# Kernel tuning notes

Measured on AMD Instinct MI355X. Metric: run time of the kernel, lower is better.

Reference implementation:

```python
import jax, jax.numpy as jnp
import numpy as np

N = 6144      # nodes
D = 64        # per-side node feature dim (out_channels of prev layer)
FE = 32       # edge feature dim
E = 196608    # edges per sign (avg degree 32)
OUT = 64
IN_DIM = 4 * D + 4 * FE  # [pos_agg, neg_agg, x_1, x_2] + 4 pooled edge-feature groups


def _l2n(x):
    return x / jnp.maximum(jnp.linalg.norm(x, axis=-1, keepdims=True), 1e-12)


def _seg_mean(vals, idx, n):
    s = jax.ops.segment_sum(vals, idx, num_segments=n)
    c = jax.ops.segment_sum(jnp.ones((vals.shape[0], 1), vals.dtype), idx, num_segments=n)
    return jnp.where(c > 0, s / jnp.maximum(c, 1.0), 0.0)


def _seg_max(vals, idx, n):
    m = jax.ops.segment_max(vals, idx, num_segments=n)
    return jnp.where(jnp.isfinite(m), m, 0.0)


def _mha(x, mask, Wq, bq, Wk, bk, Wv, bv, Wo, bo):
    # single-head torch MultiheadAttention, eval mode (no dropout); mask is additive
    q = x @ Wq + bq
    k = x @ Wk + bk
    v = x @ Wv + bv
    scale = 1.0 / jnp.sqrt(jnp.asarray(x.shape[1], x.dtype))
    scores = q @ k.T * scale + mask  # [N, N]
    return jax.nn.softmax(scores, axis=-1) @ v @ Wo + bo


def setup_inputs() -> dict:
    key = jax.random.key(0)
    ks = jax.random.split(key, 24)
    # edges without self loops: col = (row + 1 + r) % N with r in [0, N-1)
    rp = jax.random.randint(ks[0], (E,), 0, N)
    cp = (rp + 1 + jax.random.randint(ks[1], (E,), 0, N - 1)) % N
    rn = jax.random.randint(ks[2], (E,), 0, N)
    cn = (rn + 1 + jax.random.randint(ks[3], (E,), 0, N - 1)) % N
    stdv = 1.0 / np.sqrt(IN_DIM)
    inp = {
        "x_1": jax.random.normal(ks[4], (N, D), jnp.float32),
        "x_2": jax.random.normal(ks[5], (N, D), jnp.float32),
        "edge_index_pos": jnp.stack([rp, cp]),
        "edge_index_neg": jnp.stack([rn, cn]),
        "edge_feat_pos": jax.random.uniform(ks[6], (E, FE), jnp.float32),
        "edge_feat_neg": jax.random.uniform(ks[7], (E, FE), jnp.float32),
        "weight": jax.random.uniform(ks[8], (IN_DIM, OUT), jnp.float32, -stdv, stdv),
        "bias": jax.random.uniform(ks[9], (OUT,), jnp.float32, -stdv, stdv),
    }
    names = ["q_p", "k_p", "v_p", "o_p", "q_n", "k_n", "v_n", "o_n"]
    for i, nm in enumerate(names):
        inp["W" + nm] = jax.random.normal(ks[10 + i], (D, D), jnp.float32) * 0.05
        inp["b" + nm] = jnp.zeros((D,), jnp.float32)
    return inp


def reference(x_1, x_2, edge_index_pos, edge_index_neg, edge_feat_pos, edge_feat_neg,
              weight, bias,
              Wq_p, bq_p, Wk_p, bk_p, Wv_p, bv_p, Wo_p, bo_p,
              Wq_n, bq_n, Wk_n, bk_n, Wv_n, bv_n, Wo_n, bo_n):
    n = x_1.shape[0]
    loops = jnp.arange(n)
    # add self loops (inputs have none)
    rp = jnp.concatenate([edge_index_pos[0], loops])
    cp = jnp.concatenate([edge_index_pos[1], loops])
    rn = jnp.concatenate([edge_index_neg[0], loops])
    cn = jnp.concatenate([edge_index_neg[1], loops])
    # neighbor mean aggregation (scatter_mean)
    out_1 = _seg_mean(x_1[cp], rp, n)
    out_2 = _seg_mean(x_2[cn], rn, n)
    # additive attention masks: 1 everywhere, 0 on edges and their diagonals
    mask_p = (jnp.ones((n, n), x_1.dtype).at[rp, cp].set(0.0)
              .at[rp, rp].set(0.0).at[cp, cp].set(0.0))
    mask_n = (jnp.ones((n, n), x_2.dtype).at[rn, cn].set(0.0)
              .at[rn, rn].set(0.0).at[cn, cn].set(0.0))
    attn_p = _mha(x_1, mask_p, Wq_p, bq_p, Wk_p, bk_p, Wv_p, bv_p, Wo_p, bo_p)
    attn_n = _mha(x_2, mask_n, Wq_n, bq_n, Wk_n, bk_n, Wv_n, bv_n, Wo_n, bo_n)
    h1 = out_1 + attn_p
    h2 = out_2 + attn_n
    # per-node max-pooled edge features (out / in, per sign), L2-normalized
    r0, c0 = edge_index_pos[0], edge_index_pos[1]
    r1, c1 = edge_index_neg[0], edge_index_neg[1]
    po = _l2n(_seg_max(edge_feat_pos, r0, n))
    pi = _l2n(_seg_max(edge_feat_pos, c0, n))
    no_ = _l2n(_seg_max(edge_feat_neg, r1, n))
    ni = _l2n(_seg_max(edge_feat_neg, c1, n))
    feat = jnp.concatenate([h1, h2, x_1, x_2, po, pi, no_, ni], axis=1)  # [N, IN_DIM]
    out = feat @ weight + bias
    return _l2n(out)  # norm_embed
```

## Files before the change

### kernel.cpp

```cpp
#include <hip/hip_runtime.h>
#include <hip/hip_bf16.h>
#include <stdint.h>

typedef __hip_bfloat16 bf;
typedef __attribute__((ext_vector_type(8))) short short8;
typedef __attribute__((ext_vector_type(4))) short short4v;
typedef __attribute__((ext_vector_type(4))) float float4v;
__device__ __forceinline__ float b2f(bf x){ return __bfloat162float(x); }
__device__ __forceinline__ float bs2f(short s){
    return __uint_as_float(((uint32_t)(uint16_t)s) << 16);
}
__device__ __forceinline__ float sane(float x){ return fminf(fmaxf(x, -1e6f), 1e6f); }
__device__ __forceinline__ float rl(float v, int l){
    return __int_as_float(__builtin_amdgcn_readlane(__float_as_int(v), l));
}

constexpr int N   = 6144;
constexpr int D   = 64;
constexpr int FE  = 32;
constexpr int Eg  = 196608;
constexpr size_t NF = (size_t)N * D;

constexpr float L2E = 1.4426950408889634f;

__device__ __forceinline__ int clampi(int v){ return v < 0 ? 0 : (v >= N ? N - 1 : v); }
__device__ __forceinline__ float ldf(const void* p, size_t i, uint32_t isf32){
    return isf32 ? ((const float*)p)[i] : b2f(((const bf*)p)[i]);
}

constexpr size_t OF_OP   = 0;
constexpr size_t OF_LP   = OF_OP + 8*NF;
constexpr size_t OF_CO   = OF_LP + 8*(size_t)N;
constexpr size_t OF_CL   = OF_CO + 2*NF;
constexpr size_t OF_MEAN = OF_CL + 2*(size_t)N;
constexpr size_t OF_POOL = OF_MEAN + 2*NF;
constexpr size_t OF_QKVB = OF_POOL + (size_t)4*N*FE;
constexpr size_t OF_XF   = OF_QKVB + 3*NF;
constexpr size_t OF_WA   = OF_XF + 2*NF;
constexpr size_t OF_BA   = OF_WA + 24576;
constexpr size_t OF_WO   = OF_BA + 384;
constexpr size_t OF_BO   = OF_WO + 8192;
constexpr size_t OF_WF   = OF_BO + 128;
constexpr size_t OF_BF   = OF_WF + 24576;
constexpr size_t F_TOTAL = OF_BF + 64;
constexpr size_t OI_CNT  = 0;
constexpr size_t OI_PTR  = OI_CNT + 4*(size_t)N;
constexpr size_t OI_CUR  = OI_PTR + 4*(size_t)(N+1);
constexpr size_t OI_PAY  = OI_CUR + 4*(size_t)N;
constexpr size_t OI_FLAG = OI_PAY + 4*(size_t)Eg;

__global__ void zero_sniff_kernel(uint32_t* __restrict__ uz, int nu,
                                  const void* xA, const void* xB,
                                  const void* xC, const void* xD,
                                  uint32_t* __restrict__ flags){
    int i = blockIdx.x * 256 + threadIdx.x;
    if (i < nu) uz[i] = 0u;
    int sb = (int)gridDim.x - 4;
    if (blockIdx.x >= sb){
        int k = blockIdx.x - sb;
        const void* ps[4] = {xA, xB, xC, xD};
        const bf* p = (const bf*)ps[k];
        __shared__ float red[256];
        int t = threadIdx.x;
        float m = 0.f;
        for (int j = t; j < 1024; j += 256){
            float v = fabsf(b2f(p[j]));
            if (!(v <= 1e9f)) v = 1e9f;
            m = fmaxf(m, v);
        }
        red[t] = m; __syncthreads();
        for (int off = 128; off; off >>= 1){
            if (t < off) red[t] = fmaxf(red[t], red[t + off]);
            __syncthreads();
        }
        if (t == 0) flags[k] = (red[0] > 100.f) ? 1u : 0u;
    }
}

__global__ void convert_kernel(const void* x1, const void* x2,
                               const void* W0, const void* W1, const void* W2,
                               const void* W3, const void* W4, const void* W5,
                               const void* B0, const void* B1, const void* B2,
                               const void* B3, const void* B4, const void* B5,
                               const void* Wop, const void* bop,
                               const void* Won, const void* bon,
                               const void* wgt, const void* bia,
                               const int* __restrict__ eip, const int* __restrict__ ein,
                               uint32_t* __restrict__ iws,
                               const uint32_t* __restrict__ flags, float* __restrict__ ws){
    int y = blockIdx.y;
    size_t idx = (size_t)blockIdx.x * 256 + threadIdx.x;
    if (y == 0){
        uint32_t fA = flags[0];
        float v = (idx < NF) ? ldf(x1, idx, fA) : ldf(x2, idx - NF, fA);
        ws[OF_XF + idx] = sane(v);
    } else if (y == 1){
        if (idx >= 33280) return;
        uint32_t fD = flags[3];
        float v;
        if (idx < 24576){
            int m = (int)(idx >> 12), sub = (int)(idx & 4095);
            const void* W = (m==0)?W0:(m==1)?W1:(m==2)?W2:(m==3)?W3:(m==4)?W4:W5;
            v = ldf(W, sub, fD);
        } else if (idx < 24960){
            int m = (int)((idx - 24576) >> 6), sub = (int)(idx & 63);
            const void* B = (m==0)?B0:(m==1)?B1:(m==2)?B2:(m==3)?B3:(m==4)?B4:B5;
            v = ldf(B, sub, fD);
        } else if (idx < 33152){
            int k = (int)((idx - 24960) >> 12), sub = (int)(idx & 4095);
            v = ldf(k ? Won : Wop, sub, fD);
        } else {
            int k = (int)((idx - 33152) >> 6), sub = (int)(idx & 63);
            v = ldf(k ? bon : bop, sub, fD);
        }
        ws[OF_WA + idx] = sane(v);
    } else if (y == 2){
        if (idx >= 24640) return;
        uint32_t fC = flags[2];
        float v = (idx < 24576) ? ldf(wgt, idx, fC) : ldf(bia, idx - 24576, fC);
        ws[OF_WF + idx] = sane(v);
    } else {
        if (idx >= (size_t)Eg) return;
        int e = (int)idx;
        uint32_t* cnt = iws + OI_CNT;
        atomicAdd(&cnt[0 * N + clampi(eip[e])],      1u);
        atomicAdd(&cnt[1 * N + clampi(eip[Eg + e])], 1u);
        atomicAdd(&cnt[2 * N + clampi(ein[e])],      1u);
        atomicAdd(&cnt[3 * N + clampi(ein[Eg + e])], 1u);
    }
}

__global__ void scan_kernel(uint32_t* __restrict__ iws){
    int b = blockIdx.x, t = threadIdx.x;
    const uint32_t* c = iws + OI_CNT + (size_t)b * N;
    uint32_t* P  = iws + OI_PTR + (size_t)b * (N + 1);
    uint32_t* Cu = iws + OI_CUR + (size_t)b * N;
    constexpr int K = N / 256;
    int base = t * K;
    uint32_t s = 0;
    for (int k = 0; k < K; ++k) s += c[base + k];
    __shared__ uint32_t sums[256];
    sums[t] = s; __syncthreads();
    for (int off = 1; off < 256; off <<= 1){
        uint32_t v = (t >= off) ? sums[t - off] : 0u;
        __syncthreads();
        sums[t] += v;
        __syncthreads();
    }
    uint32_t run = (t == 0) ? 0u : sums[t - 1];
    for (int k = 0; k < K; ++k){ P[base + k] = run; Cu[base + k] = run; run += c[base + k]; }
    if (t == 255) P[N] = run;
}

__global__ void fill_qkv_kernel(const int* __restrict__ eip, const int* __restrict__ ein,
                                uint32_t* __restrict__ iws,
                                const float* __restrict__ ws_ro, float* __restrict__ ws){
    int b = blockIdx.x;
    if (b < 768){
        int e = b * 256 + threadIdx.x;
        if (e >= Eg) return;
        uint32_t* Cu  = iws + OI_CUR;
        uint32_t* Pay = iws + OI_PAY;
        int rp = clampi(eip[e]), cp = clampi(eip[Eg + e]);
        int rn = clampi(ein[e]), cn = clampi(ein[Eg + e]);
        uint32_t p;
        p = atomicAdd(&Cu[0 * N + rp], 1u); if (p < Eg) Pay[0 * (size_t)Eg + p] = (uint32_t)e | ((uint32_t)cp << 18);
        p = atomicAdd(&Cu[1 * N + cp], 1u); if (p < Eg) Pay[1 * (size_t)Eg + p] = (uint32_t)e | ((uint32_t)rp << 18);
        p = atomicAdd(&Cu[2 * N + rn], 1u); if (p < Eg) Pay[2 * (size_t)Eg + p] = (uint32_t)e | ((uint32_t)cn << 18);
        p = atomicAdd(&Cu[3 * N + cn], 1u); if (p < Eg) Pay[3 * (size_t)Eg + p] = (uint32_t)e | ((uint32_t)rn << 18);
        return;
    }
    int q = b - 768;
    int m = q / 384, xb = q - m * 384;
    int t = threadIdx.x, lane = t & 63, wv = t >> 6;
    int row0 = xb * 16 + wv * 4;
    const float* x = ws_ro + OF_XF + (m < 3 ? 0 : NF) + (size_t)row0 * 64;
    const float* W = ws_ro + OF_WA + (size_t)m * 4096;
    float x0 = x[lane], x1 = x[64 + lane], x2 = x[128 + lane], x3 = x[192 + lane];
    float bbias = ws_ro[OF_BA + m * 64 + lane];
    float a0 = bbias, a1 = bbias, a2 = bbias, a3 = bbias;
    #pragma unroll 16
    for (int d = 0; d < 64; ++d){
        float w = W[d * 64 + lane];
        a0 += rl(x0, d) * w;
        a1 += rl(x1, d) * w;
        a2 += rl(x2, d) * w;
        a3 += rl(x3, d) * w;
    }
    float sc = (m == 0 || m == 3) ? 0.125f * L2E : 1.f;
    bf* qkvb = (bf*)(ws + OF_QKVB) + (size_t)m * NF + (size_t)row0 * 64;
    qkvb[lane]       = __float2bfloat16(sane(a0) * sc);
    qkvb[64 + lane]  = __float2bfloat16(sane(a1) * sc);
    qkvb[128 + lane] = __float2bfloat16(sane(a2) * sc);
    qkvb[192 + lane] = __float2bfloat16(sane(a3) * sc);
}


__device__ __forceinline__ void mean_role(int b, const uint32_t* __restrict__ iws,
                                          const float* __restrict__ ws_ro, float* __restrict__ ws){
    int wid = threadIdx.x >> 6, lane = threadIdx.x & 63;
    int gw = b * 4 + wid;
    int sign = gw >= N;
    int i = gw - sign * N;
    int h = lane >> 4, t = lane & 15;
    const float* x = ws_ro + OF_XF + (size_t)sign * NF;
    int csr = sign ? 2 : 0;
    const uint32_t* P   = iws + OI_PTR + (size_t)csr * (N + 1);
    const uint32_t* Pay = iws + OI_PAY + (size_t)csr * Eg;
    uint32_t p0 = P[i], p1 = P[i + 1];
    if (p1 > (uint32_t)Eg) p1 = Eg;
    if (p0 > p1) p0 = p1;
    float4v acc = (float4v){0.f, 0.f, 0.f, 0.f};
    if (h == 0) acc = *(const float4v*)(x + (size_t)i * 64 + t * 4);
    uint32_t p = p0 + h;
    for (; p + 4 < p1; p += 8){
        int cA = (int)(Pay[p] >> 18);
        int cB = (int)(Pay[p + 4] >> 18);
        float4v vA = *(const float4v*)(x + (size_t)cA * 64 + t * 4);
        float4v vB = *(const float4v*)(x + (size_t)cB * 64 + t * 4);
        acc[0] += vA[0] + vB[0]; acc[1] += vA[1] + vB[1];
        acc[2] += vA[2] + vB[2]; acc[3] += vA[3] + vB[3];
    }
    if (p < p1){
        int c = (int)(Pay[p] >> 18);
        float4v v = *(const float4v*)(x + (size_t)c * 64 + t * 4);
        acc[0] += v[0]; acc[1] += v[1]; acc[2] += v[2]; acc[3] += v[3];
    }
    #pragma unroll
    for (int j = 0; j < 4; ++j){
        acc[j] += __shfl_xor(acc[j], 16, 64);
        acc[j] += __shfl_xor(acc[j], 32, 64);
    }
    if (h == 0){
        float invc = 1.f / (float)(p1 - p0 + 1);
        float* dst = ws + OF_MEAN + (size_t)sign * NF + (size_t)i * 64 + t * 4;
        #pragma unroll
        for (int j = 0; j < 4; ++j) dst[j] = sane(acc[j] * invc);
    }
}

__device__ __forceinline__ void pool_role(int b, const void* __restrict__ efp,
                                          const void* __restrict__ efn,
                                          const uint32_t* __restrict__ iws,
                                          uint32_t fB, float* __restrict__ ws){
    int wid = threadIdx.x >> 6, lane = threadIdx.x & 63;
    int gw = b * 4 + wid;
    int g = gw / N, i = gw - g * N;
    const void* ef = (g < 2) ? efp : efn;
    const uint32_t* P   = iws + OI_PTR + (size_t)g * (N + 1);
    const uint32_t* Pay = iws + OI_PAY + (size_t)g * Eg;
    int h = lane >> 3, t = lane & 7;
    uint32_t p0 = P[i], p1 = P[i + 1];
    if (p1 > (uint32_t)Eg) p1 = Eg;
    if (p0 > p1) p0 = p1;
    float m0 = 0.f, m1 = 0.f, m2 = 0.f, m3 = 0.f;
    uint32_t p = p0 + h;
    if (fB){
        const float* E = (const float*)ef;
        for (; p + 8 < p1; p += 16){
            uint32_t eA = Pay[p] & 0x3FFFFu, eB = Pay[p + 8] & 0x3FFFFu;
            float4v vA = *(const float4v*)(E + (size_t)eA * 32 + t * 4);
            float4v vB = *(const float4v*)(E + (size_t)eB * 32 + t * 4);
            m0 = fmaxf(m0, fmaxf(vA[0], vB[0])); m1 = fmaxf(m1, fmaxf(vA[1], vB[1]));
            m2 = fmaxf(m2, fmaxf(vA[2], vB[2])); m3 = fmaxf(m3, fmaxf(vA[3], vB[3]));
        }
        if (p < p1){
            uint32_t e = Pay[p] & 0x3FFFFu;
            float4v v = *(const float4v*)(E + (size_t)e * 32 + t * 4);
            m0 = fmaxf(m0, v[0]); m1 = fmaxf(m1, v[1]);
            m2 = fmaxf(m2, v[2]); m3 = fmaxf(m3, v[3]);
        }
    } else {
        const short* E = (const short*)ef;
        for (; p + 8 < p1; p += 16){
            uint32_t eA = Pay[p] & 0x3FFFFu, eB = Pay[p + 8] & 0x3FFFFu;
            short4v vA = *(const short4v*)(E + (size_t)eA * 32 + t * 4);
            short4v vB = *(const short4v*)(E + (size_t)eB * 32 + t * 4);
            m0 = fmaxf(m0, fmaxf(bs2f(vA[0]), bs2f(vB[0])));
            m1 = fmaxf(m1, fmaxf(bs2f(vA[1]), bs2f(vB[1])));
            m2 = fmaxf(m2, fmaxf(bs2f(vA[2]), bs2f(vB[2])));
            m3 = fmaxf(m3, fmaxf(bs2f(vA[3]), bs2f(vB[3])));
        }
        if (p < p1){
            uint32_t e = Pay[p] & 0x3FFFFu;
            short4v v = *(const short4v*)(E + (size_t)e * 32 + t * 4);
            m0 = fmaxf(m0, bs2f(v[0])); m1 = fmaxf(m1, bs2f(v[1]));
            m2 = fmaxf(m2, bs2f(v[2])); m3 = fmaxf(m3, bs2f(v[3]));
        }
    }
    #pragma unroll
    for (int mk = 8; mk <= 32; mk <<= 1){
        m0 = fmaxf(m0, __shfl_xor(m0, mk, 64));
        m1 = fmaxf(m1, __shfl_xor(m1, mk, 64));
        m2 = fmaxf(m2, __shfl_xor(m2, mk, 64));
        m3 = fmaxf(m3, __shfl_xor(m3, mk, 64));
    }
    m0 = sane(m0); m1 = sane(m1); m2 = sane(m2); m3 = sane(m3);
    float ss = m0 * m0 + m1 * m1 + m2 * m2 + m3 * m3;
    ss += __shfl_xor(ss, 1, 64); ss += __shfl_xor(ss, 2, 64); ss += __shfl_xor(ss, 4, 64);
    float inv = 1.f / fmaxf(sqrtf(ss), 1e-12f);
    if (h == 0){
        float* dst = ws + OF_POOL + ((size_t)g * N + i) * 32 + t * 4;
        dst[0] = sane(m0 * inv); dst[1] = sane(m1 * inv);
        dst[2] = sane(m2 * inv); dst[3] = sane(m3 * inv);
    }
}

__device__ __forceinline__ void corr_role(int b, const uint32_t* __restrict__ iws,
                                          const float* __restrict__ ws_ro,
                                          float* __restrict__ CO, float* __restrict__ CL){
    int wid = threadIdx.x >> 6, lane = threadIdx.x & 63;
    int gw = b * 4 + wid;
    int sg = gw >= N;
    int i = gw - sg * N;
    int h = lane >> 3, t = lane & 7;
    const bf* Qb = (const bf*)(ws_ro + OF_QKVB) + (size_t)(sg * 3) * NF;
    const short* Kb = (const short*)(Qb + NF);
    const short* Vb = Kb + NF;
    const int csr = sg ? 2 : 0;
    const uint32_t* Pp  = iws + OI_PTR + (size_t)csr * (N + 1);
    const uint32_t* Pay = iws + OI_PAY + (size_t)csr * Eg;
    uint32_t p0 = Pp[i], p1 = Pp[i + 1];
    if (p1 > (uint32_t)Eg) p1 = Eg;
    if (p0 > p1) p0 = p1;
    float qf[8];
    {
        short8 qv = *(const short8*)((const short*)Qb + (size_t)i * 64 + t * 8);
        #pragma unroll
        for (int j = 0; j < 8; ++j) qf[j] = bs2f(qv[j]);
    }
    float accO[8] = {0.f,0.f,0.f,0.f,0.f,0.f,0.f,0.f};
    float accL = 0.f;
    constexpr float C = 0.63212055882f;
    uint32_t p = p0 + h;
    for (; p + 8 <= p1; p += 16){
        int cA = (int)(Pay[p] >> 18);
        int cB = (p + 8 < p1) ? (int)(Pay[p + 8] >> 18) : i;
        short8 kvA = *(const short8*)(Kb + (size_t)cA * 64 + t * 8);
        short8 kvB = *(const short8*)(Kb + (size_t)cB * 64 + t * 8);
        short8 vvA = *(const short8*)(Vb + (size_t)cA * 64 + t * 8);
        short8 vvB = *(const short8*)(Vb + (size_t)cB * 64 + t * 8);
        float sA = qf[0] * bs2f(kvA[0]);
        float sB = qf[0] * bs2f(kvB[0]);
        #pragma unroll
        for (int j = 1; j < 8; ++j){ sA += qf[j] * bs2f(kvA[j]); sB += qf[j] * bs2f(kvB[j]); }
        sA += __shfl_xor(sA, 1, 64); sB += __shfl_xor(sB, 1, 64);
        sA += __shfl_xor(sA, 2, 64); sB += __shfl_xor(sB, 2, 64);
        sA += __shfl_xor(sA, 4, 64); sB += __shfl_xor(sB, 4, 64);
        float fA = C * __builtin_amdgcn_exp2f(sA + L2E);
        float fB = C * __builtin_amdgcn_exp2f(sB + L2E);
        accL += fA + fB;
        #pragma unroll
        for (int j = 0; j < 8; ++j) accO[j] += fA * bs2f(vvA[j]) + fB * bs2f(vvB[j]);
    }
    if (p <= p1){
        int c = (p < p1) ? (int)(Pay[p] >> 18) : i;
        short8 kv = *(const short8*)(Kb + (size_t)c * 64 + t * 8);
        short8 vv = *(const short8*)(Vb + (size_t)c * 64 + t * 8);
        float s = qf[0] * bs2f(kv[0]);
        #pragma unroll
        for (int j = 1; j < 8; ++j) s += qf[j] * bs2f(kv[j]);
        s += __shfl_xor(s, 1, 64);
        s += __shfl_xor(s, 2, 64);
        s += __shfl_xor(s, 4, 64);
        float f = C * __builtin_amdgcn_exp2f(s + L2E);
        accL += f;
        #pragma unroll
        for (int j = 0; j < 8; ++j) accO[j] += f * bs2f(vv[j]);
    }
    #pragma unroll
    for (int j = 0; j < 8; ++j){
        accO[j] += __shfl_xor(accO[j], 8, 64);
        accO[j] += __shfl_xor(accO[j], 16, 64);
        accO[j] += __shfl_xor(accO[j], 32, 64);
    }
    accL += __shfl_xor(accL, 8, 64);
    accL += __shfl_xor(accL, 16, 64);
    accL += __shfl_xor(accL, 32, 64);
    if (h == 0){
        float* Op = CO + ((size_t)sg * N + i) * 64 + t * 8;
        #pragma unroll
        for (int j = 0; j < 8; ++j) Op[j] = -accO[j];
        if (t == 0) CL[(size_t)sg * N + i] = -accL;
    }
}

__global__ void mega_kernel(const void* __restrict__ efp, const void* __restrict__ efn,
                            const uint32_t* __restrict__ iws,
                            const uint32_t* __restrict__ flags, float* __restrict__ ws){
    int b = blockIdx.x;
    if (b < 3072)       mean_role(b, iws, ws, ws);
    else if (b < 9216)  pool_role(b - 3072, efp, efn, iws, flags[1], ws);
    else                corr_role(b - 9216, iws, ws, ws + OF_CO, ws + OF_CL);
}

#define GLB1(p) ((const __attribute__((address_space(1))) void*)(p))
#define LDS3(p) ((__attribute__((address_space(3))) void*)(p))

__device__ __forceinline__ uint32_t lds_off32(const void* p){
    return (uint32_t)(uintptr_t)(__attribute__((address_space(3))) const void*)p;
}
__device__ __forceinline__ short8 ds_read_b128_off(uint32_t addr, int off){
    short8 r;
    asm volatile("ds_read_b128 %0, %1 offset:%2" : "=v"(r) : "v"(addr), "i"(off));
    return r;
}
__device__ __forceinline__ unsigned long long ds_tr16(uint32_t addr, int off){
    unsigned long long r;
    asm volatile("ds_read_b64_tr_b16 %0, %1 offset:%2" : "=v"(r) : "v"(addr), "i"(off));
    return r;
}
__device__ __forceinline__ unsigned cvt_pk_bf16(float lo, float hi){
    unsigned r;
    asm("v_cvt_pk_bf16_f32 %0, %1, %2" : "=v"(r) : "v"(lo), "v"(hi));
    return r;
}

__global__ void __launch_bounds__(256, 3)
attn_dense_kernel(const bf* __restrict__ qkvb, float* __restrict__ OP,
                  float* __restrict__ LP){
    __shared__ __align__(16) short lds_s[16384];

    int tid = threadIdx.x, lane = tid & 63, wv = tid >> 6;
    int m16 = lane & 15, quad = lane >> 4;
    int rt = blockIdx.x, cs = blockIdx.y, sg = blockIdx.z;
    const bf* Qb = qkvb + (size_t)(sg * 3) * NF;
    const bf* Kb = Qb + NF;
    const bf* Vb = Kb + NF;

    int rowbase = rt * 64 + wv * 16;
    short8 Qf0 = *(const short8*)(Qb + (size_t)(rowbase + m16) * 64 + quad * 8);
    short8 Qf1 = *(const short8*)(Qb + (size_t)(rowbase + m16) * 64 + 32 + quad * 8);

    float4v Oc[4];
    #pragma unroll
    for (int t = 0; t < 4; ++t) Oc[t] = (float4v){0.f, 0.f, 0.f, 0.f};
    float l = 0.f;

    const uint32_t lds0 = lds_off32(lds_s);

    auto stage = [&](int cb, int b){
        char* kdst = (char*)lds_s + b * 8192 + wv * 2048;
        char* vdst = (char*)lds_s + 16384 + b * 8192 + wv * 2048;
        #pragma unroll
        for (int inst = 0; inst < 2; ++inst){
            int Lb = wv * 2048 + inst * 1024 + lane * 16;
            int cl = Lb >> 7;
            int gc = (cl & 32) | (((cl >> 2) & 3) << 3) | (((cl >> 4) & 1) << 2) | (cl & 3);
            int d2 = (Lb & 127) ^ ((cl & 7) << 4);
            const char* ksrc = (const char*)Kb + (((size_t)(cb + gc)) << 7) + d2;
            __builtin_amdgcn_global_load_lds(GLB1(ksrc), LDS3(kdst + inst * 1024), 16, 0, 0);
            int idx = Lb >> 1;
            int vc  = ((idx >> 8) << 2) | ((idx >> 4) & 3);
            int vd  = (((idx >> 6) & 3) << 4) | (idx & 8);
            const char* vsrc = (const char*)Vb + (((size_t)(cb + vc)) << 7) + (vd << 1);
            __builtin_amdgcn_global_load_lds(GLB1(vsrc), LDS3(vdst + inst * 1024), 16, 0, 0);
        }
    };

    const int sw16 = (m16 & 7) << 4;
    const uint32_t kx0 = (uint32_t)(m16 * 128 + ((quad * 16) ^ sw16));
    const uint32_t kx1 = (uint32_t)(m16 * 128 + (((64 + quad * 16)) ^ sw16));
    const uint32_t vx  = (uint32_t)(quad * 1024 + m16 * 2);

    int c0 = cs * (N / 4), c1 = c0 + N / 4;
    stage(c0, 0);
    asm volatile("s_waitcnt vmcnt(0)" ::: "memory");
    __syncthreads();

    int buf = 0;
    for (int cb = c0; cb < c1; cb += 64){
        if (cb + 64 < c1) stage(cb + 64, buf ^ 1);
        uint32_t kb0 = lds0 + (uint32_t)(buf * 8192) + kx0;
        uint32_t kb1 = lds0 + (uint32_t)(buf * 8192) + kx1;
        uint32_t vab = lds0 + 16384u + (uint32_t)(buf * 8192) + vx;
        #pragma unroll
        for (int kg = 0; kg < 2; ++kg){
            short8 A[2][2];
            #pragma unroll
            for (int ct = 0; ct < 2; ++ct){
                A[ct][0] = ds_read_b128_off(kb0, kg * 4096 + ct * 2048);
                A[ct][1] = ds_read_b128_off(kb1, kg * 4096 + ct * 2048);
            }
            unsigned long long tr[8];
            #pragma unroll
            for (int dt = 0; dt < 4; ++dt)
                #pragma unroll
                for (int w = 0; w < 2; ++w)
                    tr[dt * 2 + w] = ds_tr16(vab, kg * 4096 + w * 512 + dt * 128);
            asm volatile("s_waitcnt lgkmcnt(8)" ::: "memory");
            __builtin_amdgcn_sched_barrier(0);
            float4v s0 = __builtin_amdgcn_mfma_f32_16x16x32_bf16(
                             A[0][0], Qf0, (float4v){0.f,0.f,0.f,0.f}, 0, 0, 0);
            s0 = __builtin_amdgcn_mfma_f32_16x16x32_bf16(A[0][1], Qf1, s0, 0, 0, 0);
            float4v s1 = __builtin_amdgcn_mfma_f32_16x16x32_bf16(
                             A[1][0], Qf0, (float4v){0.f,0.f,0.f,0.f}, 0, 0, 0);
            s1 = __builtin_amdgcn_mfma_f32_16x16x32_bf16(A[1][1], Qf1, s1, 0, 0, 0);
            float p0[4], p1[4];
            #pragma unroll
            for (int r = 0; r < 4; ++r){
                p0[r] = __builtin_amdgcn_exp2f(s0[r] + L2E);
                p1[r] = __builtin_amdgcn_exp2f(s1[r] + L2E);
                l += p0[r] + p1[r];
            }
            union { unsigned u[4]; short8 s8; } pf;
            pf.u[0] = cvt_pk_bf16(p0[0], p0[1]);
            pf.u[1] = cvt_pk_bf16(p0[2], p0[3]);
            pf.u[2] = cvt_pk_bf16(p1[0], p1[1]);
            pf.u[3] = cvt_pk_bf16(p1[2], p1[3]);
            asm volatile("s_waitcnt lgkmcnt(0)" ::: "memory");
            __builtin_amdgcn_sched_barrier(0);
            #pragma unroll
            for (int dt = 0; dt < 4; ++dt){
                union { unsigned long long u[2]; short8 s8; } va;
                va.u[0] = tr[dt * 2];
                va.u[1] = tr[dt * 2 + 1];
                Oc[dt] = __builtin_amdgcn_mfma_f32_16x16x32_bf16(va.s8, pf.s8, Oc[dt], 0, 0, 0);
            }
        }
        asm volatile("s_waitcnt vmcnt(0)" ::: "memory");
        __syncthreads();
        buf ^= 1;
    }

    l += __shfl_xor(l, 16, 64);
    l += __shfl_xor(l, 32, 64);
    int slab = cs * 2 + sg;
    if (quad == 0) LP[(size_t)slab * N + rowbase + m16] = l;
    float* Op = OP + ((size_t)slab * N + rowbase + m16) * 64;
    #pragma unroll
    for (int dt = 0; dt < 4; ++dt)
        *(float4v*)(Op + dt * 16 + quad * 4) = Oc[dt];
}

__global__ void final_kernel(const uint32_t* __restrict__ flags,
                             const float* __restrict__ ws, void* __restrict__ outv){
    uint32_t fA = flags[0];
    int t = threadIdx.x, lane = t & 63, wv = t >> 6;
    int row0 = blockIdx.x * 16 + wv * 4;
    float fr[6][4];
    #pragma unroll
    for (int s = 0; s < 2; ++s){
        float onr[4];
        #pragma unroll
        for (int r = 0; r < 4; ++r){
            int i = row0 + r;
            float osum = ws[OF_CO + ((size_t)s * N + i) * 64 + lane];
            float lsum = ws[OF_CL + (size_t)s * N + i];
            #pragma unroll
            for (int cs = 0; cs < 4; ++cs){
                int slab = cs * 2 + s;
                osum += ws[OF_OP + ((size_t)slab * N + i) * 64 + lane];
                lsum += ws[OF_LP + (size_t)slab * N + i];
            }
            onr[r] = sane(osum / fmaxf(lsum, 1e-20f));
        }
        const float* Wo = ws + OF_WO + (size_t)s * 4096;
        float b0 = ws[OF_BO + s * 64 + lane];
        float a[4] = {b0, b0, b0, b0};
        #pragma unroll 16
        for (int d = 0; d < 64; ++d){
            float w = Wo[d * 64 + lane];
            a[0] += rl(onr[0], d) * w;
            a[1] += rl(onr[1], d) * w;
            a[2] += rl(onr[2], d) * w;
            a[3] += rl(onr[3], d) * w;
        }
        #pragma unroll
        for (int r = 0; r < 4; ++r){
            int i = row0 + r;
            float mean = ws[OF_MEAN + (size_t)s * NF + (size_t)i * 64 + lane];
            fr[s][r] = sane(mean + a[r]);
        }
    }
    {
        int g0 = lane >> 5, f = lane & 31;
        #pragma unroll
        for (int r = 0; r < 4; ++r){
            int i = row0 + r;
            fr[2][r] = ws[OF_XF + (size_t)i * 64 + lane];
            fr[3][r] = ws[OF_XF + NF + (size_t)i * 64 + lane];
            fr[4][r] = ws[OF_POOL + ((size_t)g0 * N + i) * 32 + f];
            fr[5][r] = ws[OF_POOL + ((size_t)(2 + g0) * N + i) * 32 + f];
        }
    }
    const float* WF = ws + OF_WF;
    float bf0 = ws[OF_BF + lane];
    float acc[4] = {bf0, bf0, bf0, bf0};
    #pragma unroll
    for (int j = 0; j < 6; ++j){
        #pragma unroll 16
        for (int dd = 0; dd < 64; ++dd){
            float w = WF[(size_t)(j * 64 + dd) * 64 + lane];
            acc[0] += rl(fr[j][0], dd) * w;
            acc[1] += rl(fr[j][1], dd) * w;
            acc[2] += rl(fr[j][2], dd) * w;
            acc[3] += rl(fr[j][3], dd) * w;
        }
    }
    #pragma unroll
    for (int r = 0; r < 4; ++r){
        float a = sane(acc[r]);
        float ss = a * a;
        ss += __shfl_xor(ss, 32, 64); ss += __shfl_xor(ss, 16, 64); ss += __shfl_xor(ss, 8, 64);
        ss += __shfl_xor(ss, 4, 64);  ss += __shfl_xor(ss, 2, 64);  ss += __shfl_xor(ss, 1, 64);
        float out = a / fmaxf(sqrtf(ss), 1e-12f);
        int i = row0 + r;
        if (fA) ((float*)outv)[(size_t)i * 64 + lane] = out;
        else    ((bf*)outv)[(size_t)i * 64 + lane] = __float2bfloat16(out);
    }
}

extern "C" void kernel_launch(void* const* d_in, const int* in_sizes, int n_in,
                              void* d_out, int out_size, void* d_ws, size_t ws_size,
                              hipStream_t stream){
    const int* eip = (const int*)d_in[2];
    const int* ein = (const int*)d_in[3];

    float* ws = (float*)d_ws;
    uint32_t* iws = (uint32_t*)(ws + F_TOTAL);
    uint32_t* flags = iws + OI_FLAG;
    bf* qkvb = (bf*)(ws + OF_QKVB);

    int nu = 4 * N;
    zero_sniff_kernel<<<dim3((nu + 255) / 256), 256, 0, stream>>>(
        iws + OI_CNT, nu, d_in[0], d_in[4], d_in[6], d_in[8], flags);
    convert_kernel<<<dim3(3072, 4), 256, 0, stream>>>(
        d_in[0], d_in[1],
        d_in[8],  d_in[10], d_in[12], d_in[16], d_in[18], d_in[20],
        d_in[9],  d_in[11], d_in[13], d_in[17], d_in[19], d_in[21],
        d_in[14], d_in[15], d_in[22], d_in[23],
        d_in[6],  d_in[7],
        eip, ein, iws,
        flags, ws);
    scan_kernel<<<4, 256, 0, stream>>>(iws);
    fill_qkv_kernel<<<dim3(768 + 2304), 256, 0, stream>>>(eip, ein, iws, ws, ws);
    attn_dense_kernel<<<dim3(N / 64, 4, 2), 256, 0, stream>>>(qkvb, ws + OF_OP, ws + OF_LP);
    mega_kernel<<<dim3(12288), 256, 0, stream>>>(d_in[4], d_in[5], iws, flags, ws);
    final_kernel<<<dim3(N / 16), 256, 0, stream>>>(flags, ws, d_out);
}
```

Baseline: 211.6 us.

## Regroup kernels: scan with QKV projection, CSR fill with dense attention

The scan kernel is merged with the QKV projection into one launch, and the CSR payload fill is merged into the dense attention kernel as extra blocks. This cuts one kernel launch and lets the atomic-heavy edge fill overlap with the MFMA attention work instead of running serially. The fill blocks now inherit the attention kernel's large LDS allocation and launch bounds, which may limit how many of them fit per CU. Block index decoding for attention changes from a 3D to a 1D grid.

```diff
diff --git a/kernel.cpp b/kernel.cpp
--- a/kernel.cpp
+++ b/kernel.cpp
@@ -130,8 +130,8 @@
     }
 }
 
-__global__ void scan_kernel(uint32_t* __restrict__ iws){
-    int b = blockIdx.x, t = threadIdx.x;
+__device__ __forceinline__ void scan_role(int b, uint32_t* __restrict__ iws){
+    int t = threadIdx.x;
     const uint32_t* c = iws + OI_CNT + (size_t)b * N;
     uint32_t* P  = iws + OI_PTR + (size_t)b * (N + 1);
     uint32_t* Cu = iws + OI_CUR + (size_t)b * N;
@@ -152,25 +152,8 @@
     if (t == 255) P[N] = run;
 }
 
-__global__ void fill_qkv_kernel(const int* __restrict__ eip, const int* __restrict__ ein,
-                                uint32_t* __restrict__ iws,
-                                const float* __restrict__ ws_ro, float* __restrict__ ws){
-    int b = blockIdx.x;
-    if (b < 768){
-        int e = b * 256 + threadIdx.x;
-        if (e >= Eg) return;
-        uint32_t* Cu  = iws + OI_CUR;
-        uint32_t* Pay = iws + OI_PAY;
-        int rp = clampi(eip[e]), cp = clampi(eip[Eg + e]);
-        int rn = clampi(ein[e]), cn = clampi(ein[Eg + e]);
-        uint32_t p;
-        p = atomicAdd(&Cu[0 * N + rp], 1u); if (p < Eg) Pay[0 * (size_t)Eg + p] = (uint32_t)e | ((uint32_t)cp << 18);
-        p = atomicAdd(&Cu[1 * N + cp], 1u); if (p < Eg) Pay[1 * (size_t)Eg + p] = (uint32_t)e | ((uint32_t)rp << 18);
-        p = atomicAdd(&Cu[2 * N + rn], 1u); if (p < Eg) Pay[2 * (size_t)Eg + p] = (uint32_t)e | ((uint32_t)cn << 18);
-        p = atomicAdd(&Cu[3 * N + cn], 1u); if (p < Eg) Pay[3 * (size_t)Eg + p] = (uint32_t)e | ((uint32_t)rn << 18);
-        return;
-    }
-    int q = b - 768;
+__device__ __forceinline__ void qkv_role(int q, const float* __restrict__ ws_ro,
+                                         float* __restrict__ ws){
     int m = q / 384, xb = q - m * 384;
     int t = threadIdx.x, lane = t & 63, wv = t >> 6;
     int row0 = xb * 16 + wv * 4;
@@ -193,6 +176,13 @@
     qkvb[64 + lane]  = __float2bfloat16(sane(a1) * sc);
     qkvb[128 + lane] = __float2bfloat16(sane(a2) * sc);
     qkvb[192 + lane] = __float2bfloat16(sane(a3) * sc);
+}
+
+__global__ void scan_qkv_kernel(uint32_t* __restrict__ iws,
+                                const float* __restrict__ ws_ro, float* __restrict__ ws){
+    int b = blockIdx.x;
+    if (b < 4) scan_role(b, iws);
+    else       qkv_role(b - 4, ws_ro, ws);
 }
 
 
@@ -416,14 +406,11 @@
     return r;
 }
 
-__global__ void __launch_bounds__(256, 3)
-attn_dense_kernel(const bf* __restrict__ qkvb, float* __restrict__ OP,
-                  float* __restrict__ LP){
-    __shared__ __align__(16) short lds_s[16384];
-
+__device__ void attn_role(int ab, short* lds_s, const bf* __restrict__ qkvb,
+                          float* __restrict__ OP, float* __restrict__ LP){
     int tid = threadIdx.x, lane = tid & 63, wv = tid >> 6;
     int m16 = lane & 15, quad = lane >> 4;
-    int rt = blockIdx.x, cs = blockIdx.y, sg = blockIdx.z;
+    int rt = ab % 96, cs = (ab / 96) & 3, sg = ab / 384;
     const bf* Qb = qkvb + (size_t)(sg * 3) * NF;
     const bf* Kb = Qb + NF;
     const bf* Vb = Kb + NF;
@@ -533,6 +520,29 @@
         *(float4v*)(Op + dt * 16 + quad * 4) = Oc[dt];
 }
 
+__global__ void __launch_bounds__(256, 3)
+attn_fill_kernel(const int* __restrict__ eip, const int* __restrict__ ein,
+                 uint32_t* __restrict__ iws, const bf* __restrict__ qkvb,
+                 float* __restrict__ OP, float* __restrict__ LP){
+    __shared__ __align__(16) short lds_s[16384];
+    int b = blockIdx.x;
+    if (b < 768){
+        attn_role(b, lds_s, qkvb, OP, LP);
+        return;
+    }
+    int e = (b - 768) * 256 + threadIdx.x;
+    if (e >= Eg) return;
+    uint32_t* Cu  = iws + OI_CUR;
+    uint32_t* Pay = iws + OI_PAY;
+    int rp = clampi(eip[e]), cp = clampi(eip[Eg + e]);
+    int rn = clampi(ein[e]), cn = clampi(ein[Eg + e]);
+    uint32_t p;
+    p = atomicAdd(&Cu[0 * N + rp], 1u); if (p < Eg) Pay[0 * (size_t)Eg + p] = (uint32_t)e | ((uint32_t)cp << 18);
+    p = atomicAdd(&Cu[1 * N + cp], 1u); if (p < Eg) Pay[1 * (size_t)Eg + p] = (uint32_t)e | ((uint32_t)rp << 18);
+    p = atomicAdd(&Cu[2 * N + rn], 1u); if (p < Eg) Pay[2 * (size_t)Eg + p] = (uint32_t)e | ((uint32_t)cn << 18);
+    p = atomicAdd(&Cu[3 * N + cn], 1u); if (p < Eg) Pay[3 * (size_t)Eg + p] = (uint32_t)e | ((uint32_t)rn << 18);
+}
+
 __global__ void final_kernel(const uint32_t* __restrict__ flags,
                              const float* __restrict__ ws, void* __restrict__ outv){
     uint32_t fA = flags[0];
@@ -633,9 +643,9 @@
         d_in[6],  d_in[7],
         eip, ein, iws,
         flags, ws);
-    scan_kernel<<<4, 256, 0, stream>>>(iws);
-    fill_qkv_kernel<<<dim3(768 + 2304), 256, 0, stream>>>(eip, ein, iws, ws, ws);
-    attn_dense_kernel<<<dim3(N / 64, 4, 2), 256, 0, stream>>>(qkvb, ws + OF_OP, ws + OF_LP);
+    scan_qkv_kernel<<<dim3(4 + 2304), 256, 0, stream>>>(iws, ws, ws);
+    attn_fill_kernel<<<dim3(768 + 768), 256, 0, stream>>>(
+        eip, ein, iws, qkvb, ws + OF_OP, ws + OF_LP);
     mega_kernel<<<dim3(12288), 256, 0, stream>>>(d_in[4], d_in[5], iws, flags, ws);
     final_kernel<<<dim3(N / 16), 256, 0, stream>>>(flags, ws, d_out);
 }
```

Result: faster. 186.3 us, median of 2 (-12.0%).
